# Kernel tuning notes

Hardware: AMD Instinct MI355X
Metric: run time of the kernel (lower is better)

## Reference

```python
import jax, jax.numpy as jnp
import numpy as np

N = 100000

def gcn_conv(x, W, b, src, dst, n):
    # PyG GCNConv: h = x W; add self-loops; norm = deg^-1/2[src]*deg^-1/2[dst]; scatter-add; + bias
    h = x @ W                                   # [N, out]
    deg = jax.ops.segment_sum(jnp.ones_like(dst, dtype=h.dtype), dst, num_segments=n)
    dinv = jnp.where(deg > 0, jax.lax.rsqrt(jnp.maximum(deg, 1e-12)), 0.0)
    norm = dinv[src] * dinv[dst]                # [E+N]
    msgs = h[src] * norm[:, None]               # gather + scale
    out = jax.ops.segment_sum(msgs, dst, num_segments=n)  # scatter-add
    return out + b

def setup_inputs() -> dict:
    key = jax.random.key(0)
    k1, k2, k3, k4, k5, k6 = jax.random.split(key, 6)
    E = 3200000
    F_in, H, C = 512, 50, 40
    x = jax.random.normal(k1, (N, F_in), dtype=jnp.float32)
    edge_index = jax.random.randint(k2, (2, E), 0, N, dtype=jnp.int32)
    # Glorot-style init for linear weights, zero bias (PyG default)
    W1 = jax.random.normal(k3, (F_in, H), dtype=jnp.float32) * (1.0 / np.sqrt(F_in))
    b1 = jnp.zeros((H,), dtype=jnp.float32)
    W2 = jax.random.normal(k4, (H, C), dtype=jnp.float32) * (1.0 / np.sqrt(H))
    b2 = jnp.zeros((C,), dtype=jnp.float32)
    return {"x": x, "W1": W1, "b1": b1, "W2": W2, "b2": b2, "edge_index": edge_index}

def reference(x, W1, b1, W2, b2, edge_index):
    n = x.shape[0]
    loops = jnp.arange(n, dtype=edge_index.dtype)
    src = jnp.concatenate([edge_index[0], loops])
    dst = jnp.concatenate([edge_index[1], loops])
    h = gcn_conv(x, W1, b1, src, dst, n)
    h = jax.nn.relu(h)
    # dropout identity in eval mode
    h = gcn_conv(h, W2, b2, src, dst, n)
    return jax.nn.log_softmax(h, axis=1)
```

## Files before the change

kernel.cpp:

```cpp
#include <hip/hip_runtime.h>
#include <hip/hip_bf16.h>
#include <math.h>

#define F_IN 512
#define H_DIM 50
#define C_DIM 40
#define H_STR 56
#define C_STR 40
#define NB_SHIFT 9
#define NB_SIZE (1 << NB_SHIFT)
#define PB_EDGES 4096

typedef __bf16 bf16x8 __attribute__((ext_vector_type(8)));
typedef __bf16 bf16x4 __attribute__((ext_vector_type(4)));
typedef float f32x4 __attribute__((ext_vector_type(4)));



__global__ void prep_wt_kernel(const float* __restrict__ W1, __bf16* __restrict__ wt,
                               int* __restrict__ bcur, int cap,
                               __bf16* __restrict__ h1b, __bf16* __restrict__ h2b, int N) {
    if (blockIdx.x == 0) {
        bcur[threadIdx.x] = threadIdx.x * cap;
        if (threadIdx.x < H_STR) h1b[(long)N * H_STR + threadIdx.x] = (__bf16)0.0f;
        if (threadIdx.x < C_STR) h2b[(long)N * C_STR + threadIdx.x] = (__bf16)0.0f;
    }
    int i = blockIdx.x * 256 + threadIdx.x;
    int n = i >> 9, k = i & 511;
    wt[n * 512 + k] = (n < H_DIM) ? (__bf16)W1[k * H_DIM + n] : (__bf16)0.0f;
}

__global__ __launch_bounds__(256) void partition_kernel(
    const int* __restrict__ src, const int* __restrict__ dst,
    int* __restrict__ bcur, int* __restrict__ ebuf, int E, int cap) {
    __shared__ int lcnt[256];
    __shared__ int lbase[256];
    const int t = threadIdx.x;
    lcnt[t] = 0;
    __syncthreads();
    const long b0 = (long)blockIdx.x * PB_EDGES;
    int s[16], d[16], rk[16];
    #pragma unroll
    for (int ci = 0; ci < 4; ++ci) {
        long e = b0 + ci * 1024 + t * 4;
        const int j0 = ci * 4;
        if (e + 3 < E) {
            int4 d4 = *(const int4*)(dst + e);
            int4 s4 = *(const int4*)(src + e);
            s[j0] = s4.x; s[j0 + 1] = s4.y; s[j0 + 2] = s4.z; s[j0 + 3] = s4.w;
            d[j0] = d4.x; d[j0 + 1] = d4.y; d[j0 + 2] = d4.z; d[j0 + 3] = d4.w;
        } else {
            #pragma unroll
            for (int j = 0; j < 4; ++j) {
                if (e + j < E) { s[j0 + j] = src[e + j]; d[j0 + j] = dst[e + j]; }
                else           { s[j0 + j] = 0;          d[j0 + j] = -1; }
            }
        }
        #pragma unroll
        for (int j = 0; j < 4; ++j)
            rk[j0 + j] = (d[j0 + j] >= 0) ? atomicAdd(&lcnt[d[j0 + j] >> NB_SHIFT], 1) : -1;
    }
    __syncthreads();
    lbase[t] = lcnt[t] ? atomicAdd(&bcur[t], lcnt[t]) : 0;
    __syncthreads();
    #pragma unroll
    for (int j = 0; j < 16; ++j)
        if (rk[j] >= 0) {
            int bk = d[j] >> NB_SHIFT;
            int idx = lbase[bk] + rk[j];
            if (idx < (bk + 1) * cap)
                ebuf[idx] = (s[j] << NB_SHIFT) | (d[j] & (NB_SIZE - 1));
        }
}

__global__ __launch_bounds__(256) void bucket_csr_kernel(
    const int* __restrict__ ebuf, const int* __restrict__ bcur,
    int* __restrict__ cnt, int* __restrict__ rowptr, float* __restrict__ dinv,
    int* __restrict__ adj, int N, int cap) {
    __shared__ int h[NB_SIZE];
    __shared__ int wsum[4];
    const int t = threadIdx.x, lane = t & 63, wv = t >> 6;
    const int b = blockIdx.x, v0 = b << NB_SHIFT;
    const int gbase = b * cap;
    const int cb = min(bcur[b] - gbase, cap);
    h[2 * t] = 0; h[2 * t + 1] = 0;
    __syncthreads();
    const int* ep = ebuf + gbase;
    for (int i = t; i < cb; i += 256)
        atomicAdd(&h[ep[i] & (NB_SIZE - 1)], 1);
    __syncthreads();
    const int a0 = h[2 * t], a1 = h[2 * t + 1];
    const int p0 = (a0 + 31) & ~31, p1 = (a1 + 31) & ~31;
    const int tsum = p0 + p1;
    int incl = tsum;
    #pragma unroll
    for (int off = 1; off < 64; off <<= 1) {
        int u = __shfl_up(incl, off, 64);
        if (lane >= off) incl += u;
    }
    if (lane == 63) wsum[wv] = incl;
    __syncthreads();
    int woff = 0;
    #pragma unroll
    for (int w = 0; w < 3; ++w) woff += (w < wv) ? wsum[w] : 0;
    const int ex = woff + incl - tsum;
    const int r0 = gbase + ex, r1 = r0 + p0;
    h[2 * t] = r0; h[2 * t + 1] = r1;
    const int i0 = v0 + 2 * t, i1 = i0 + 1;
    if (i0 < N) { rowptr[i0] = r0; cnt[i0] = a0; dinv[i0] = rsqrtf((float)(a0 + 1)); }
    if (i1 < N) { rowptr[i1] = r1; cnt[i1] = a1; dinv[i1] = rsqrtf((float)(a1 + 1)); }
    __syncthreads();
    const int nq = cb >> 2;
    for (int q = t; q < nq; q += 256) {
        int4 e4 = *(const int4*)(ep + q * 4);
        int q0 = atomicAdd(&h[e4.x & (NB_SIZE - 1)], 1);
        int q1 = atomicAdd(&h[e4.y & (NB_SIZE - 1)], 1);
        int q2 = atomicAdd(&h[e4.z & (NB_SIZE - 1)], 1);
        int q3 = atomicAdd(&h[e4.w & (NB_SIZE - 1)], 1);
        adj[q0] = e4.x >> NB_SHIFT;
        adj[q1] = e4.y >> NB_SHIFT;
        adj[q2] = e4.z >> NB_SHIFT;
        adj[q3] = e4.w >> NB_SHIFT;
    }
    const int rem = cb & 3;
    if (t < rem) {
        int e = ep[nq * 4 + t];
        int p = atomicAdd(&h[e & (NB_SIZE - 1)], 1);
        adj[p] = e >> NB_SHIFT;
    }
    for (int k = r0 + a0; k < r0 + p0; ++k) adj[k] = N;
    for (int k = r1 + a1; k < r1 + p1; ++k) adj[k] = N;
}


#define G1_BM 128
#define G1_BK 32
#define A_LDW 40

__device__ __forceinline__ bf16x4 pack4(float4 a) {
    bf16x4 r;
    r[0] = (__bf16)a.x; r[1] = (__bf16)a.y; r[2] = (__bf16)a.z; r[3] = (__bf16)a.w;
    return r;
}

__global__ __launch_bounds__(256) void gemm1_mfma_kernel(
    const float* __restrict__ x, const __bf16* __restrict__ wt,
    const float* __restrict__ dinv, __bf16* __restrict__ h1b, int N) {
    __shared__ __bf16 As[2][G1_BM * A_LDW];
    __shared__ __bf16 Bs[2][64 * A_LDW];

    const int t = threadIdx.x;
    const int wv = t >> 6, ln = t & 63;
    const int q = ln >> 4, l16 = ln & 15;
    const int row0 = blockIdx.x * G1_BM;

    f32x4 acc[2][4];
    #pragma unroll
    for (int a = 0; a < 2; ++a)
        #pragma unroll
        for (int b = 0; b < 4; ++b) acc[a][b] = (f32x4){0.f, 0.f, 0.f, 0.f};

    const int c4 = t & 7;
    const int r0 = t >> 3;
    const float* xp[4];
    #pragma unroll
    for (int j = 0; j < 4; ++j) {
        int gr = row0 + r0 + 32 * j;
        int rc = (gr < N) ? gr : (N - 1);
        xp[j] = x + (long)rc * F_IN + c4 * 4;
    }
    const int bc = t & 3;
    const int bn = t >> 2;
    const __bf16* wb = wt + bn * 512 + bc * 8;

    float4 xv[4];
    uint4 w8;

    #pragma unroll
    for (int j = 0; j < 4; ++j) xv[j] = *(const float4*)(xp[j]);
    w8 = *(const uint4*)(wb);
    #pragma unroll
    for (int j = 0; j < 4; ++j)
        *(bf16x4*)&As[0][(r0 + 32 * j) * A_LDW + c4 * 4] = pack4(xv[j]);
    *(bf16x8*)&Bs[0][bn * A_LDW + bc * 8] = *(bf16x8*)&w8;
    __syncthreads();

    #pragma unroll 1
    for (int tt = 0; tt < F_IN / G1_BK; ++tt) {
        int b = tt & 1;
        if (tt < F_IN / G1_BK - 1) {
            #pragma unroll
            for (int j = 0; j < 4; ++j)
                xv[j] = *(const float4*)(xp[j] + (tt + 1) * G1_BK);
            w8 = *(const uint4*)(wb + (tt + 1) * G1_BK);
        }
        bf16x8 af[2], bfr[4];
        #pragma unroll
        for (int mt = 0; mt < 2; ++mt)
            af[mt] = *(const bf16x8*)&As[b][(wv * 32 + mt * 16 + l16) * A_LDW + q * 8];
        #pragma unroll
        for (int nt = 0; nt < 4; ++nt)
            bfr[nt] = *(const bf16x8*)&Bs[b][(nt * 16 + l16) * A_LDW + q * 8];
        #pragma unroll
        for (int mt = 0; mt < 2; ++mt)
            #pragma unroll
            for (int nt = 0; nt < 4; ++nt)
                acc[mt][nt] = __builtin_amdgcn_mfma_f32_16x16x32_bf16(
                    af[mt], bfr[nt], acc[mt][nt], 0, 0, 0);
        if (tt < F_IN / G1_BK - 1) {
            int nb = b ^ 1;
            #pragma unroll
            for (int j = 0; j < 4; ++j)
                *(bf16x4*)&As[nb][(r0 + 32 * j) * A_LDW + c4 * 4] = pack4(xv[j]);
            *(bf16x8*)&Bs[nb][bn * A_LDW + bc * 8] = *(bf16x8*)&w8;
        }
        __syncthreads();
    }

    #pragma unroll
    for (int mt = 0; mt < 2; ++mt) {
        int rbase = row0 + wv * 32 + mt * 16 + q * 4;
        #pragma unroll
        for (int i = 0; i < 4; ++i) {
            int r = rbase + i;
            if (r < N) {
                float dv = dinv[r];
                #pragma unroll
                for (int nt = 0; nt < 4; ++nt) {
                    int col = nt * 16 + l16;
                    if (col < H_STR)
                        h1b[(long)r * H_STR + col] = (__bf16)(acc[mt][nt][i] * dv);
                }
            }
        }
    }
}


__global__ __launch_bounds__(256) void gather1_gemm2_kernel(
    const int* __restrict__ rowptr, const int* __restrict__ cnt,
    const int* __restrict__ adj,
    const float* __restrict__ dinv, const __bf16* __restrict__ h1b,
    const float* __restrict__ b1, const float* __restrict__ W2,
    __bf16* __restrict__ h2b, int N) {
    __shared__ float w2s[H_DIM][C_DIM];
    __shared__ float b1s[64];
    __shared__ float r1s[4][64];
    for (int i = threadIdx.x; i < H_DIM * C_DIM; i += 256)
        w2s[i / C_DIM][i % C_DIM] = W2[i];
    if (threadIdx.x < 64)
        b1s[threadIdx.x] = (threadIdx.x < H_DIM) ? b1[threadIdx.x] : 0.0f;
    __syncthreads();

    const int lane = threadIdx.x & 63;
    const int wv = threadIdx.x >> 6;
    const int n = blockIdx.x * 4 + wv;
    const int c = lane & 7;
    const int cc = (c < 7) ? c : 6;
    const int g = lane >> 3;
    const char* h1p = (const char*)h1b + cc * 16;

    float acc[8];
    #pragma unroll
    for (int i = 0; i < 8; ++i) acc[i] = 0.0f;

    if (g == 0) {
        bf16x8 v = *(const bf16x8*)(h1p + __umul24((unsigned)n, (unsigned)(H_STR * 2)));
        #pragma unroll
        for (int i = 0; i < 8; ++i) acc[i] += (float)v[i];
    }

    const int c0 = cnt[n];
    const int c0p = (c0 + 31) & ~31;
    const int* row = adj + rowptr[n];
    for (int base = 0; base < c0p; base += 32) {
        int i0 = row[base + g];
        int i1 = row[base + g + 8];
        int i2 = row[base + g + 16];
        int i3 = row[base + g + 24];
        bf16x8 v0 = *(const bf16x8*)(h1p + __umul24((unsigned)i0, (unsigned)(H_STR * 2)));
        bf16x8 v1 = *(const bf16x8*)(h1p + __umul24((unsigned)i1, (unsigned)(H_STR * 2)));
        bf16x8 v2 = *(const bf16x8*)(h1p + __umul24((unsigned)i2, (unsigned)(H_STR * 2)));
        bf16x8 v3 = *(const bf16x8*)(h1p + __umul24((unsigned)i3, (unsigned)(H_STR * 2)));
        #pragma unroll
        for (int i = 0; i < 8; ++i) {
            acc[i] += (float)v0[i];
            acc[i] += (float)v1[i];
            acc[i] += (float)v2[i];
            acc[i] += (float)v3[i];
        }
    }

    #pragma unroll
    for (int i = 0; i < 8; ++i) {
        acc[i] += __shfl_xor(acc[i], 8, 64);
        acc[i] += __shfl_xor(acc[i], 16, 64);
        acc[i] += __shfl_xor(acc[i], 32, 64);
    }
    const float dv = dinv[n];
    if (g == 0) {
        #pragma unroll
        for (int i = 0; i < 8; ++i)
            r1s[wv][c * 8 + i] = fmaxf(acc[i] * dv + b1s[c * 8 + i], 0.0f);
    }
    __syncthreads();

    if (lane < C_DIM) {
        float a2 = 0.0f;
        #pragma unroll
        for (int k = 0; k < H_DIM; ++k) a2 += r1s[wv][k] * w2s[k][lane];
        h2b[(long)n * C_STR + lane] = (__bf16)(a2 * dv);
    }
}


__global__ __launch_bounds__(256) void gather2_kernel(
    const int* __restrict__ rowptr, const int* __restrict__ cnt,
    const int* __restrict__ adj,
    const float* __restrict__ dinv, const __bf16* __restrict__ h2b,
    const float* __restrict__ b2, float* __restrict__ out2, int N) {
    __shared__ float sc[4][64];
    const int lane = threadIdx.x & 63;
    const int wv = threadIdx.x >> 6;
    const int n = blockIdx.x * 4 + wv;
    const int c = lane & 7;
    const int cc = (c < 5) ? c : 4;
    const int g = lane >> 3;
    const char* h2p = (const char*)h2b + cc * 16;

    float acc[8];
    #pragma unroll
    for (int i = 0; i < 8; ++i) acc[i] = 0.0f;

    if (g == 0) {
        bf16x8 v = *(const bf16x8*)(h2p + __umul24((unsigned)n, (unsigned)(C_STR * 2)));
        #pragma unroll
        for (int i = 0; i < 8; ++i) acc[i] += (float)v[i];
    }

    const int c0 = cnt[n];
    const int c0p = (c0 + 31) & ~31;
    const int* row = adj + rowptr[n];
    for (int base = 0; base < c0p; base += 32) {
        int i0 = row[base + g];
        int i1 = row[base + g + 8];
        int i2 = row[base + g + 16];
        int i3 = row[base + g + 24];
        bf16x8 v0 = *(const bf16x8*)(h2p + __umul24((unsigned)i0, (unsigned)(C_STR * 2)));
        bf16x8 v1 = *(const bf16x8*)(h2p + __umul24((unsigned)i1, (unsigned)(C_STR * 2)));
        bf16x8 v2 = *(const bf16x8*)(h2p + __umul24((unsigned)i2, (unsigned)(C_STR * 2)));
        bf16x8 v3 = *(const bf16x8*)(h2p + __umul24((unsigned)i3, (unsigned)(C_STR * 2)));
        #pragma unroll
        for (int i = 0; i < 8; ++i) {
            acc[i] += (float)v0[i];
            acc[i] += (float)v1[i];
            acc[i] += (float)v2[i];
            acc[i] += (float)v3[i];
        }
    }

    #pragma unroll
    for (int i = 0; i < 8; ++i) {
        acc[i] += __shfl_xor(acc[i], 8, 64);
        acc[i] += __shfl_xor(acc[i], 16, 64);
        acc[i] += __shfl_xor(acc[i], 32, 64);
    }
    if (g == 0) {
        #pragma unroll
        for (int i = 0; i < 8; ++i) sc[wv][c * 8 + i] = acc[i];
    }
    __syncthreads();

    const bool valid = lane < C_DIM;
    float v = valid ? (sc[wv][lane] * dinv[n] + b2[lane]) : -INFINITY;

    float m = v;
    #pragma unroll
    for (int off = 1; off < 64; off <<= 1)
        m = fmaxf(m, __shfl_xor(m, off, 64));
    float ex = valid ? __expf(v - m) : 0.0f;
    #pragma unroll
    for (int off = 1; off < 64; off <<= 1)
        ex += __shfl_xor(ex, off, 64);
    float ls = __logf(ex) + m;
    if (valid) out2[(long)n * C_DIM + lane] = v - ls;
}


extern "C" void kernel_launch(void* const* d_in, const int* in_sizes, int n_in,
                              void* d_out, int out_size, void* d_ws, size_t ws_size,
                              hipStream_t stream) {
    const float* x  = (const float*)d_in[0];
    const float* W1 = (const float*)d_in[1];
    const float* b1 = (const float*)d_in[2];
    const float* W2 = (const float*)d_in[3];
    const float* b2 = (const float*)d_in[4];
    const int* ei   = (const int*)d_in[5];

    const int N = in_sizes[0] / F_IN;
    const int E = in_sizes[5] / 2;
    const int* src = ei;
    const int* dst = ei + E;
    float* out2 = (float*)d_out;

    const int nbuck = (N + NB_SIZE - 1) >> NB_SHIFT;
    const int CAP = (int)((((long)2 * E / nbuck) + 255) & ~255L);

    int* wsw = (int*)d_ws;
    long o = 0;
    int*    cnt    = wsw + o;  o += N;
    int*    bcur   = wsw + o;  o += 256;
    int*    rowptr = wsw + o;  o += N;
    int*    adj    = wsw + o;  o += (long)nbuck * CAP;
    int*    ebuf   = wsw + o;  o += (long)nbuck * CAP;
    float*  dinv   = (float*)(wsw + o); o += N;
    __bf16* wt     = (__bf16*)(wsw + o); o += (64 * 512) / 2;
    __bf16* h1b    = (__bf16*)(wsw + o); o += (long)(N + 1) * H_STR / 2 + 4;
    __bf16* h2b    = (__bf16*)(wsw + o); o += (long)(N + 1) * C_STR / 2 + 4;

    const int BT = 256;
    const int gP = (E + PB_EDGES - 1) / PB_EDGES;

    prep_wt_kernel<<<128, 256, 0, stream>>>(W1, wt, bcur, CAP, h1b, h2b, N);
    partition_kernel<<<gP, BT, 0, stream>>>(src, dst, bcur, ebuf, E, CAP);
    bucket_csr_kernel<<<nbuck, BT, 0, stream>>>(ebuf, bcur, cnt, rowptr, dinv, adj, N, CAP);

    gemm1_mfma_kernel<<<(N + G1_BM - 1) / G1_BM, 256, 0, stream>>>(x, wt, dinv, h1b, N);
    gather1_gemm2_kernel<<<N / 4, 256, 0, stream>>>(rowptr, cnt, adj, dinv, h1b, b1, W2, h2b, N);
    gather2_kernel<<<N / 4, 256, 0, stream>>>(rowptr, cnt, adj, dinv, h2b, b2, out2, N);
}
```

Before: 542.7 us.

## Load GEMM1 MFMA operands directly from global memory, dropping LDS staging

```diff
diff --git a/kernel.cpp b/kernel.cpp
--- a/kernel.cpp
+++ b/kernel.cpp
@@ -12,7 +12,6 @@
 #define PB_EDGES 4096
 
 typedef __bf16 bf16x8 __attribute__((ext_vector_type(8)));
-typedef __bf16 bf16x4 __attribute__((ext_vector_type(4)));
 typedef float f32x4 __attribute__((ext_vector_type(4)));
 
 
@@ -134,87 +133,69 @@
 
 
 #define G1_BM 128
-#define G1_BK 32
-#define A_LDW 40
-
-__device__ __forceinline__ bf16x4 pack4(float4 a) {
-    bf16x4 r;
+
+__device__ __forceinline__ bf16x8 pack8(float4 a, float4 b) {
+    bf16x8 r;
     r[0] = (__bf16)a.x; r[1] = (__bf16)a.y; r[2] = (__bf16)a.z; r[3] = (__bf16)a.w;
+    r[4] = (__bf16)b.x; r[5] = (__bf16)b.y; r[6] = (__bf16)b.z; r[7] = (__bf16)b.w;
     return r;
 }
 
 __global__ __launch_bounds__(256) void gemm1_mfma_kernel(
     const float* __restrict__ x, const __bf16* __restrict__ wt,
     const float* __restrict__ dinv, __bf16* __restrict__ h1b, int N) {
-    __shared__ __bf16 As[2][G1_BM * A_LDW];
-    __shared__ __bf16 Bs[2][64 * A_LDW];
-
     const int t = threadIdx.x;
     const int wv = t >> 6, ln = t & 63;
     const int q = ln >> 4, l16 = ln & 15;
     const int row0 = blockIdx.x * G1_BM;
 
+    int ra0 = row0 + wv * 32 + l16;
+    int ra1 = ra0 + 16;
+    ra0 = (ra0 < N) ? ra0 : (N - 1);
+    ra1 = (ra1 < N) ? ra1 : (N - 1);
+    const float4* xa0 = (const float4*)(x + (long)ra0 * F_IN + q * 8);
+    const float4* xa1 = (const float4*)(x + (long)ra1 * F_IN + q * 8);
+    const uint4* wb0 = (const uint4*)(wt + (0 * 16 + l16) * 512 + q * 8);
+    const uint4* wb1 = (const uint4*)(wt + (1 * 16 + l16) * 512 + q * 8);
+    const uint4* wb2 = (const uint4*)(wt + (2 * 16 + l16) * 512 + q * 8);
+    const uint4* wb3 = (const uint4*)(wt + (3 * 16 + l16) * 512 + q * 8);
+
     f32x4 acc[2][4];
     #pragma unroll
     for (int a = 0; a < 2; ++a)
         #pragma unroll
         for (int b = 0; b < 4; ++b) acc[a][b] = (f32x4){0.f, 0.f, 0.f, 0.f};
 
-    const int c4 = t & 7;
-    const int r0 = t >> 3;
-    const float* xp[4];
-    #pragma unroll
-    for (int j = 0; j < 4; ++j) {
-        int gr = row0 + r0 + 32 * j;
-        int rc = (gr < N) ? gr : (N - 1);
-        xp[j] = x + (long)rc * F_IN + c4 * 4;
-    }
-    const int bc = t & 3;
-    const int bn = t >> 2;
-    const __bf16* wb = wt + bn * 512 + bc * 8;
-
-    float4 xv[4];
-    uint4 w8;
-
-    #pragma unroll
-    for (int j = 0; j < 4; ++j) xv[j] = *(const float4*)(xp[j]);
-    w8 = *(const uint4*)(wb);
-    #pragma unroll
-    for (int j = 0; j < 4; ++j)
-        *(bf16x4*)&As[0][(r0 + 32 * j) * A_LDW + c4 * 4] = pack4(xv[j]);
-    *(bf16x8*)&Bs[0][bn * A_LDW + bc * 8] = *(bf16x8*)&w8;
-    __syncthreads();
-
-    #pragma unroll 1
-    for (int tt = 0; tt < F_IN / G1_BK; ++tt) {
-        int b = tt & 1;
-        if (tt < F_IN / G1_BK - 1) {
-            #pragma unroll
-            for (int j = 0; j < 4; ++j)
-                xv[j] = *(const float4*)(xp[j] + (tt + 1) * G1_BK);
-            w8 = *(const uint4*)(wb + (tt + 1) * G1_BK);
-        }
-        bf16x8 af[2], bfr[4];
-        #pragma unroll
-        for (int mt = 0; mt < 2; ++mt)
-            af[mt] = *(const bf16x8*)&As[b][(wv * 32 + mt * 16 + l16) * A_LDW + q * 8];
-        #pragma unroll
-        for (int nt = 0; nt < 4; ++nt)
-            bfr[nt] = *(const bf16x8*)&Bs[b][(nt * 16 + l16) * A_LDW + q * 8];
-        #pragma unroll
-        for (int mt = 0; mt < 2; ++mt)
-            #pragma unroll
-            for (int nt = 0; nt < 4; ++nt)
-                acc[mt][nt] = __builtin_amdgcn_mfma_f32_16x16x32_bf16(
-                    af[mt], bfr[nt], acc[mt][nt], 0, 0, 0);
-        if (tt < F_IN / G1_BK - 1) {
-            int nb = b ^ 1;
-            #pragma unroll
-            for (int j = 0; j < 4; ++j)
-                *(bf16x4*)&As[nb][(r0 + 32 * j) * A_LDW + c4 * 4] = pack4(xv[j]);
-            *(bf16x8*)&Bs[nb][bn * A_LDW + bc * 8] = *(bf16x8*)&w8;
-        }
-        __syncthreads();
+    float4 a00 = xa0[0], a01 = xa0[1];
+    float4 a10 = xa1[0], a11 = xa1[1];
+    uint4 b0 = wb0[0], b1 = wb1[0], b2 = wb2[0], b3 = wb3[0];
+
+    #pragma unroll
+    for (int tt = 0; tt < F_IN / 32; ++tt) {
+        float4 n00, n01, n10, n11;
+        uint4 nb0, nb1, nb2, nb3;
+        if (tt < F_IN / 32 - 1) {
+            n00 = xa0[(tt + 1) * 8];     n01 = xa0[(tt + 1) * 8 + 1];
+            n10 = xa1[(tt + 1) * 8];     n11 = xa1[(tt + 1) * 8 + 1];
+            nb0 = wb0[(tt + 1) * 4];     nb1 = wb1[(tt + 1) * 4];
+            nb2 = wb2[(tt + 1) * 4];     nb3 = wb3[(tt + 1) * 4];
+        }
+        bf16x8 af0 = pack8(a00, a01);
+        bf16x8 af1 = pack8(a10, a11);
+        bf16x8 bf0 = *(bf16x8*)&b0, bf1 = *(bf16x8*)&b1;
+        bf16x8 bf2 = *(bf16x8*)&b2, bf3 = *(bf16x8*)&b3;
+        acc[0][0] = __builtin_amdgcn_mfma_f32_16x16x32_bf16(af0, bf0, acc[0][0], 0, 0, 0);
+        acc[0][1] = __builtin_amdgcn_mfma_f32_16x16x32_bf16(af0, bf1, acc[0][1], 0, 0, 0);
+        acc[0][2] = __builtin_amdgcn_mfma_f32_16x16x32_bf16(af0, bf2, acc[0][2], 0, 0, 0);
+        acc[0][3] = __builtin_amdgcn_mfma_f32_16x16x32_bf16(af0, bf3, acc[0][3], 0, 0, 0);
+        acc[1][0] = __builtin_amdgcn_mfma_f32_16x16x32_bf16(af1, bf0, acc[1][0], 0, 0, 0);
+        acc[1][1] = __builtin_amdgcn_mfma_f32_16x16x32_bf16(af1, bf1, acc[1][1], 0, 0, 0);
+        acc[1][2] = __builtin_amdgcn_mfma_f32_16x16x32_bf16(af1, bf2, acc[1][2], 0, 0, 0);
+        acc[1][3] = __builtin_amdgcn_mfma_f32_16x16x32_bf16(af1, bf3, acc[1][3], 0, 0, 0);
+        if (tt < F_IN / 32 - 1) {
+            a00 = n00; a01 = n01; a10 = n10; a11 = n11;
+            b0 = nb0; b1 = nb1; b2 = nb2; b3 = nb3;
+        }
     }
 
     #pragma unroll
```

Result: no change. 553.3 us (+2.0%).
